# Kernel optimization log

Measured on AMD Instinct MI355X. Metric: run time of the kernel, lower is better.

## Reference

```python
import jax, jax.numpy as jnp
import numpy as np

B, CIN, COUT, N, K = 8, 128, 128, 2000, 16
IN_EPS = 1e-3   # InstanceNorm2d eps in module
BN_EPS = 1e-5   # BatchNorm2d default eps


def conv1x1(x, w, b):
    # x: [B,C,H,W], w: [O,C], b: [O]
    return jnp.einsum('bchw,oc->bohw', x, w) + b[None, :, None, None]


def setup_inputs() -> dict:
    key = jax.random.key(0)
    ks = jax.random.split(key, 12)
    s = 0.05
    return {
        'x_row':   jax.random.normal(ks[0], (B, COUT, N, 1), jnp.float32),
        'x_local': jax.random.normal(ks[1], (B, CIN, N, K), jnp.float32),
        'w0': jax.random.normal(ks[2], (COUT, CIN), jnp.float32) * s,
        'b0': jax.random.normal(ks[3], (COUT,), jnp.float32) * s,
        'bn_g': jnp.ones((COUT,), jnp.float32),
        'bn_b': jnp.zeros((COUT,), jnp.float32),
        'wq': jax.random.normal(ks[4], (COUT, COUT), jnp.float32) * s,
        'bq': jax.random.normal(ks[5], (COUT,), jnp.float32) * s,
        'wk': jax.random.normal(ks[6], (COUT, COUT), jnp.float32) * s,
        'bk': jax.random.normal(ks[7], (COUT,), jnp.float32) * s,
        'wv': jax.random.normal(ks[8], (COUT, COUT), jnp.float32) * s,
        'bv': jax.random.normal(ks[9], (COUT,), jnp.float32) * s,
        'gamma1': jnp.ones((1,), jnp.float32),
    }


def reference(x_row, x_local, w0, b0, bn_g, bn_b, wq, bq, wk, bk, wv, bv, gamma1):
    # att1: Conv1x1 -> InstanceNorm2d(eps=1e-3, no affine) -> BatchNorm2d (train-mode batch stats) -> ReLU
    h = conv1x1(x_local, w0, b0)                       # [B,C,N,K]
    mu = jnp.mean(h, axis=(2, 3), keepdims=True)
    var = jnp.var(h, axis=(2, 3), keepdims=True)
    h = (h - mu) * jax.lax.rsqrt(var + IN_EPS)
    bmu = jnp.mean(h, axis=(0, 2, 3), keepdims=True)
    bvar = jnp.var(h, axis=(0, 2, 3), keepdims=True)
    h = (h - bmu) * jax.lax.rsqrt(bvar + BN_EPS)
    h = h * bn_g[None, :, None, None] + bn_b[None, :, None, None]
    h = jax.nn.relu(h)

    q = conv1x1(h, wq, bq)
    k = conv1x1(h, wk, bk)
    v = conv1x1(h, wv, bv)
    att = jax.nn.softmax(q * k, axis=3)                # softmax over neighbor axis
    out_local = jnp.sum(att * v, axis=3, keepdims=True)  # [B,C,N,1]
    return x_row + gamma1 * out_local
```

## Files before the change

kernel.cpp:

```cpp
#include <hip/hip_runtime.h>
#include <math.h>

#define NB 8
#define NC 128
#define NPOS 2000
#define NK 32000
#define IN_EPS 1e-3f
#define BN_EPS 1e-5f

typedef short bf16x8 __attribute__((ext_vector_type(8)));
typedef _Float16 f16x8 __attribute__((ext_vector_type(8)));
typedef float f32x4 __attribute__((ext_vector_type(4)));
typedef unsigned short ushort_t;
typedef unsigned int uint_t;

#define XSTRIDE 136

#define WSF_SUMP  0
#define WSF_SQP   32768
#define WSF_ALPHA 65536
#define WSF_BETA  66560
#define WSB_WEIGHTS 270336
#define WSB_H     401408
#define WS_NEEDED ((size_t)WSB_H + (size_t)NB * NK * XSTRIDE * 2)

__device__ __forceinline__ f32x4 mfma_bf16(bf16x8 a, bf16x8 b, f32x4 c) {
  return __builtin_amdgcn_mfma_f32_16x16x32_bf16(a, b, c, 0, 0, 0);
}
__device__ __forceinline__ f32x4 mfma_f16(f16x8 a, f16x8 b, f32x4 c) {
  return __builtin_amdgcn_mfma_f32_16x16x32_f16(a, b, c, 0, 0, 0);
}

__device__ __forceinline__ ushort_t f2bf(float f) {
  unsigned u = __float_as_uint(f);
  return (ushort_t)((u + 0x7FFFu + ((u >> 16) & 1u)) >> 16);
}
__device__ __forceinline__ ushort_t f2h(float f) {
  union { _Float16 h; ushort_t u; } cv;
  cv.h = (_Float16)f;
  return cv.u;
}
__device__ __forceinline__ float h2f(ushort_t u) {
  union { _Float16 h; ushort_t u; } cv;
  cv.u = u;
  return (float)cv.h;
}
__device__ __forceinline__ uint_t pk2h(float a, float b) {
  auto h = __builtin_amdgcn_cvt_pkrtz(a, b);
  return __builtin_bit_cast(uint_t, h);
}

template <int ALL_F16>
__global__ __launch_bounds__(256) void k_prep(const float* __restrict__ w0,
    const float* __restrict__ wq, const float* __restrict__ wk,
    const float* __restrict__ wv, ushort_t* __restrict__ wb) {
  int idx = blockIdx.x * 256 + threadIdx.x;
  int m = idx >> 14;
  int e = idx & 16383;
  const float* src = (m == 0) ? w0 : (m == 1) ? wq : (m == 2) ? wk : wv;
  float v = src[e];
  wb[m * 16384 + e] = ALL_F16 ? f2h(v) : f2bf(v);
}

__device__ __forceinline__ void stage_xt128(const float* __restrict__ xb,
                                            ushort_t* __restrict__ xt, int tid) {
  const int col = tid & 127;
  const int hi = tid >> 7;
  const float* p = xb + col;
#pragma unroll
  for (int i = 0; i < 8; ++i) {
    const int c0 = hi * 64 + i * 8;
    ushort_t u[8] __attribute__((aligned(16)));
#pragma unroll
    for (int j = 0; j < 8; ++j) u[j] = f2bf(p[(size_t)(c0 + j) * NK]);
    *(uint4*)(xt + col * XSTRIDE + c0) = *(const uint4*)u;
  }
}

__device__ __forceinline__ void stage_xt64(const float* __restrict__ xb,
                                           ushort_t* __restrict__ xt, int tid) {
  const int col = tid & 63;
  const int hi = tid >> 6;
  const float* p = xb + col;
#pragma unroll
  for (int i = 0; i < 4; ++i) {
    const int c0 = hi * 32 + i * 8;
    ushort_t u[8] __attribute__((aligned(16)));
#pragma unroll
    for (int j = 0; j < 8; ++j) u[j] = f2bf(p[(size_t)(c0 + j) * NK]);
    *(uint4*)(xt + col * XSTRIDE + c0) = *(const uint4*)u;
  }
}

__device__ __forceinline__ void stage_xt64_f16(const float* __restrict__ xb,
                                               ushort_t* __restrict__ xt, int tid) {
  const int col = tid & 63;
  const int hi = tid >> 6;
  const float* p = xb + col;
#pragma unroll
  for (int r = 0; r < 2; ++r) {
    const int c0 = hi * 32 + r * 16;
    float v[16];
#pragma unroll
    for (int j = 0; j < 16; ++j) v[j] = p[(size_t)(c0 + j) * NK];
    uint_t u[8] __attribute__((aligned(16)));
#pragma unroll
    for (int j = 0; j < 8; ++j) u[j] = pk2h(v[2 * j], v[2 * j + 1]);
    *(uint4*)(xt + col * XSTRIDE + c0) = *(const uint4*)u;
    *(uint4*)(xt + col * XSTRIDE + c0 + 8) = *(const uint4*)(u + 4);
  }
}

__global__ __launch_bounds__(256, 6) void k_stats2(const float* __restrict__ x,
    const ushort_t* __restrict__ w0b, float* __restrict__ sumP,
    float* __restrict__ sqP, ushort_t* __restrict__ hg) {
  __shared__ ushort_t xt[64 * XSTRIDE] __attribute__((aligned(16)));
  __shared__ float ssum[128], ssq[128];
  const int b = blockIdx.y;
  const int tid = threadIdx.x;
  stage_xt64_f16(x + (size_t)b * NC * NK + (size_t)blockIdx.x * 64, xt, tid);
  __syncthreads();
  const int lane = tid & 63, w = tid >> 6;
  const int m = lane & 15, quad = lane >> 4;

  uint2 hreg[8];

#pragma unroll
  for (int p = 0; p < 2; ++p) {
    const int ch0 = (w + p * 4) * 16;
    f16x8 wf[4];
#pragma unroll
    for (int kb = 0; kb < 4; ++kb)
      wf[kb] = *(const f16x8*)(w0b + (ch0 + m) * 128 + kb * 32 + quad * 8);
    float s0 = 0.f, s1 = 0.f, s2 = 0.f, s3 = 0.f;
    float q0 = 0.f, q1 = 0.f, q2 = 0.f, q3 = 0.f;
#pragma unroll
    for (int t = 0; t < 4; ++t) {
      const ushort_t* xr = xt + (t * 16 + m) * XSTRIDE;
      f32x4 acc = {0.f, 0.f, 0.f, 0.f};
#pragma unroll
      for (int kb = 0; kb < 4; ++kb) {
        f16x8 bx = *(const f16x8*)(xr + kb * 32 + quad * 8);
        acc = mfma_f16(wf[kb], bx, acc);
      }
      const ushort_t u0 = f2h(acc[0]), u1 = f2h(acc[1]);
      const ushort_t u2 = f2h(acc[2]), u3 = f2h(acc[3]);
      uint2 pk;
      pk.x = (uint_t)u0 | ((uint_t)u1 << 16);
      pk.y = (uint_t)u2 | ((uint_t)u3 << 16);
      hreg[p * 4 + t] = pk;
      const float r0 = h2f(u0), r1 = h2f(u1), r2 = h2f(u2), r3 = h2f(u3);
      s0 += r0; s1 += r1; s2 += r2; s3 += r3;
      q0 = fmaf(r0, r0, q0); q1 = fmaf(r1, r1, q1);
      q2 = fmaf(r2, r2, q2); q3 = fmaf(r3, r3, q3);
    }
#pragma unroll
    for (int d = 1; d < 16; d <<= 1) {
      s0 += __shfl_xor(s0, d); s1 += __shfl_xor(s1, d);
      s2 += __shfl_xor(s2, d); s3 += __shfl_xor(s3, d);
      q0 += __shfl_xor(q0, d); q1 += __shfl_xor(q1, d);
      q2 += __shfl_xor(q2, d); q3 += __shfl_xor(q3, d);
    }
    if (m == 0) {
      ssum[ch0 + quad * 4 + 0] = s0; ssum[ch0 + quad * 4 + 1] = s1;
      ssum[ch0 + quad * 4 + 2] = s2; ssum[ch0 + quad * 4 + 3] = s3;
      ssq[ch0 + quad * 4 + 0] = q0; ssq[ch0 + quad * 4 + 1] = q1;
      ssq[ch0 + quad * 4 + 2] = q2; ssq[ch0 + quad * 4 + 3] = q3;
    }
  }
  __syncthreads();

#pragma unroll
  for (int p = 0; p < 2; ++p) {
    const int ch0 = (w + p * 4) * 16;
#pragma unroll
    for (int t = 0; t < 4; ++t)
      *(uint2*)(xt + (t * 16 + m) * XSTRIDE + ch0 + quad * 4) = hreg[p * 4 + t];
  }
  __syncthreads();

  {
    const uint4* src = (const uint4*)xt;
    uint4* dst =
        (uint4*)(hg + ((size_t)b * NK + (size_t)blockIdx.x * 64) * XSTRIDE);
#pragma unroll
    for (int i = 0; i < 4; ++i) dst[i * 256 + tid] = src[i * 256 + tid];
    if (tid < 64) dst[1024 + tid] = src[1024 + tid];
  }

  if (tid < 128) {
    const int bucket = blockIdx.x & 31;
    atomicAdd(&sumP[bucket * 1024 + b * 128 + tid], ssum[tid]);
    atomicAdd(&sqP[bucket * 1024 + b * 128 + tid], ssq[tid]);
  }
}

__global__ void k_fold(const float* __restrict__ ws_in, const float* __restrict__ bn_g,
                       const float* __restrict__ bn_b, float* __restrict__ alpha,
                       float* __restrict__ beta) {
  int c = threadIdx.x;
  const float* sumP = ws_in + WSF_SUMP;
  const float* sqP = ws_in + WSF_SQP;
  float var[NB], muv[NB];
  float bvar = 0.f;
#pragma unroll 1
  for (int b = 0; b < NB; ++b) {
    float s = 0.f, q = 0.f;
#pragma unroll
    for (int k = 0; k < 32; ++k) {
      s += sumP[k * 1024 + b * 128 + c];
      q += sqP[k * 1024 + b * 128 + c];
    }
    float mu = s * (1.f / NK);
    float v = q * (1.f / NK) - mu * mu;
    muv[b] = mu;
    var[b] = v;
    bvar += v / (v + IN_EPS);
  }
  bvar *= 0.125f;
  float s2 = rsqrtf(bvar + BN_EPS);
  float g = bn_g[c], bb = bn_b[c];
#pragma unroll
  for (int b = 0; b < NB; ++b) {
    float a = rsqrtf(var[b] + IN_EPS) * s2 * g;
    alpha[b * 128 + c] = a;
    beta[b * 128 + c] = bb - muv[b] * a;
  }
}

__device__ __forceinline__ uint_t norm2(uint_t hv, float a0, float a1, float c0,
                                        float c1) {
  float lo = h2f((ushort_t)(hv & 0xffffu));
  float hi = h2f((ushort_t)(hv >> 16));
  return pk2h(fmaxf(fmaf(lo, a0, c0), 0.f), fmaxf(fmaf(hi, a1, c1), 0.f));
}

__global__ __launch_bounds__(256, 6) void k_fused2(
    const ushort_t* __restrict__ hg, const float* __restrict__ x_row,
    const ushort_t* __restrict__ wb, const float* __restrict__ alpha,
    const float* __restrict__ beta, const float* __restrict__ bq,
    const float* __restrict__ bk, const float* __restrict__ bv,
    const float* __restrict__ g1p, float* __restrict__ out) {
  __shared__ ushort_t xt[64 * XSTRIDE] __attribute__((aligned(16)));
  __shared__ float souts[128 * 5];
  const int b = blockIdx.y;
  const int tid = threadIdx.x;
  const int lane = tid & 63, w = tid >> 6;

  const size_t oi = ((size_t)b * NC + tid) * NPOS + blockIdx.x * 4;
  float4 xr_early;
  if (tid < 128) xr_early = *(const float4*)(x_row + oi);

  {
    const uint4* src =
        (const uint4*)(hg + ((size_t)b * NK + (size_t)blockIdx.x * 64) * XSTRIDE);
    uint4* dst = (uint4*)xt;
    const float* ap = alpha + b * 128;
    const float* bp = beta + b * 128;
#pragma unroll
    for (int i = 0; i < 5; ++i) {
      if (i < 4 || tid < 64) {
        const int j = i * 256 + tid;
        uint4 v = src[j];
        const int c = j % 17;
        if (c < 16) {
          const int ch = c * 8;
          const float4 a0 = *(const float4*)(ap + ch);
          const float4 a1 = *(const float4*)(ap + ch + 4);
          const float4 c0 = *(const float4*)(bp + ch);
          const float4 c1 = *(const float4*)(bp + ch + 4);
          v.x = norm2(v.x, a0.x, a0.y, c0.x, c0.y);
          v.y = norm2(v.y, a0.z, a0.w, c0.z, c0.w);
          v.z = norm2(v.z, a1.x, a1.y, c1.x, c1.y);
          v.w = norm2(v.w, a1.z, a1.w, c1.z, c1.w);
        }
        dst[j] = v;
      }
    }
  }
  const float g1 = g1p[0];
  __syncthreads();

  const int m = lane & 15, quad = lane >> 4;
  const ushort_t* wqb = wb + 16384;
  const ushort_t* wkb = wb + 32768;
  const ushort_t* wvb = wb + 49152;
#pragma unroll 1
  for (int p = 0; p < 2; ++p) {
    const int ch0 = (w + p * 4) * 16;
    f16x8 wqf[4], wkf[4], wvf[4];
#pragma unroll
    for (int kb = 0; kb < 4; ++kb) {
      wqf[kb] = *(const f16x8*)(wqb + (ch0 + m) * 128 + kb * 32 + quad * 8);
      wkf[kb] = *(const f16x8*)(wkb + (ch0 + m) * 128 + kb * 32 + quad * 8);
      wvf[kb] = *(const f16x8*)(wvb + (ch0 + m) * 128 + kb * 32 + quad * 8);
    }
    const float bqv = bq[ch0 + m];
    const float bkv = bk[ch0 + m];
    const float bvv = bv[ch0 + m];
#pragma unroll 1
    for (int t = 0; t < 4; ++t) {
      const ushort_t* hr = xt + (t * 16 + m) * XSTRIDE;
      f16x8 af[4];
#pragma unroll
      for (int kb = 0; kb < 4; ++kb)
        af[kb] = *(const f16x8*)(hr + kb * 32 + quad * 8);
      f32x4 qa = {0.f, 0.f, 0.f, 0.f};
      f32x4 ka = {0.f, 0.f, 0.f, 0.f};
#pragma unroll
      for (int kb = 0; kb < 4; ++kb) qa = mfma_f16(af[kb], wqf[kb], qa);
#pragma unroll
      for (int kb = 0; kb < 4; ++kb) ka = mfma_f16(af[kb], wkf[kb], ka);
      float p0 = (qa[0] + bqv) * (ka[0] + bkv);
      float p1 = (qa[1] + bqv) * (ka[1] + bkv);
      float p2 = (qa[2] + bqv) * (ka[2] + bkv);
      float p3 = (qa[3] + bqv) * (ka[3] + bkv);
      float mx = fmaxf(fmaxf(p0, p1), fmaxf(p2, p3));
      mx = fmaxf(mx, __shfl_xor(mx, 16));
      mx = fmaxf(mx, __shfl_xor(mx, 32));
      float e0 = __expf(p0 - mx), e1 = __expf(p1 - mx);
      float e2 = __expf(p2 - mx), e3 = __expf(p3 - mx);
      float sm = (e0 + e1) + (e2 + e3);
      sm += __shfl_xor(sm, 16);
      sm += __shfl_xor(sm, 32);
      f32x4 va = {0.f, 0.f, 0.f, 0.f};
#pragma unroll
      for (int kb = 0; kb < 4; ++kb) va = mfma_f16(af[kb], wvf[kb], va);
      float r0 = e0 * va[0] + e1 * va[1] + e2 * va[2] + e3 * va[3];
      r0 += __shfl_xor(r0, 16);
      r0 += __shfl_xor(r0, 32);
      if (quad == 0) souts[(ch0 + m) * 5 + t] = r0 / sm + bvv;
    }
  }
  __syncthreads();

  if (tid < 128) {
    const float* sp = souts + tid * 5;
    float4 o;
    o.x = xr_early.x + g1 * sp[0];
    o.y = xr_early.y + g1 * sp[1];
    o.z = xr_early.z + g1 * sp[2];
    o.w = xr_early.w + g1 * sp[3];
    *(float4*)(out + oi) = o;
  }
}

__global__ __launch_bounds__(256, 4) void k_stats1(const float* __restrict__ x,
    const ushort_t* __restrict__ w0b, float* __restrict__ sumP,
    float* __restrict__ sqP) {
  __shared__ ushort_t xt[128 * XSTRIDE];
  __shared__ float ssum[128], ssq[128];
  const int b = blockIdx.y;
  const int tid = threadIdx.x;
  stage_xt128(x + (size_t)b * NC * NK + (size_t)blockIdx.x * 128, xt, tid);
  __syncthreads();
  const int lane = tid & 63, w = tid >> 6;
  const int m = lane & 15, quad = lane >> 4;

#pragma unroll 1
  for (int p = 0; p < 2; ++p) {
    const int ch0 = (w + p * 4) * 16;
    bf16x8 wf[4];
#pragma unroll
    for (int kb = 0; kb < 4; ++kb)
      wf[kb] = *(const bf16x8*)(w0b + (ch0 + m) * 128 + kb * 32 + quad * 8);
    float s = 0.f, q2 = 0.f;
#pragma unroll 2
    for (int t = 0; t < 8; ++t) {
      const ushort_t* xr = xt + (t * 16 + m) * XSTRIDE;
      f32x4 acc = {0.f, 0.f, 0.f, 0.f};
#pragma unroll
      for (int kb = 0; kb < 4; ++kb) {
        bf16x8 af = *(const bf16x8*)(xr + kb * 32 + quad * 8);
        acc = mfma_bf16(af, wf[kb], acc);
      }
      s += (acc[0] + acc[1]) + (acc[2] + acc[3]);
      q2 += (acc[0] * acc[0] + acc[1] * acc[1]) +
            (acc[2] * acc[2] + acc[3] * acc[3]);
    }
    s += __shfl_xor(s, 16);
    s += __shfl_xor(s, 32);
    q2 += __shfl_xor(q2, 16);
    q2 += __shfl_xor(q2, 32);
    if (quad == 0) {
      ssum[ch0 + m] = s;
      ssq[ch0 + m] = q2;
    }
  }
  __syncthreads();
  if (tid < 128) {
    const int bucket = blockIdx.x & 31;
    atomicAdd(&sumP[bucket * 1024 + b * 128 + tid], ssum[tid]);
    atomicAdd(&sqP[bucket * 1024 + b * 128 + tid], ssq[tid]);
  }
}

__global__ __launch_bounds__(256, 4) void k_fused1(const float* __restrict__ x,
    const float* __restrict__ x_row, const ushort_t* __restrict__ wb,
    const float* __restrict__ alpha, const float* __restrict__ beta,
    const float* __restrict__ bq, const float* __restrict__ bk,
    const float* __restrict__ bv, const float* __restrict__ g1p,
    float* __restrict__ out) {
  __shared__ ushort_t xt[64 * XSTRIDE];
  __shared__ ushort_t ht[64 * XSTRIDE];
  __shared__ float souts[128 * 5];
  const int b = blockIdx.y;
  const int tid = threadIdx.x;
  stage_xt64(x + (size_t)b * NC * NK + (size_t)blockIdx.x * 64, xt, tid);
  const float g1 = g1p[0];
  __syncthreads();
  const int lane = tid & 63, w = tid >> 6;
  const int m = lane & 15, quad = lane >> 4;
  const ushort_t* w0b = wb;
  const ushort_t* wqb = wb + 16384;
  const ushort_t* wkb = wb + 32768;
  const ushort_t* wvb = wb + 49152;

#pragma unroll 1
  for (int p = 0; p < 2; ++p) {
    const int ch0 = (w + p * 4) * 16;
    bf16x8 wf[4];
#pragma unroll
    for (int kb = 0; kb < 4; ++kb)
      wf[kb] = *(const bf16x8*)(w0b + (ch0 + m) * 128 + kb * 32 + quad * 8);
    const float4 av = *(const float4*)(alpha + b * 128 + ch0 + quad * 4);
    const float4 bev = *(const float4*)(beta + b * 128 + ch0 + quad * 4);
#pragma unroll
    for (int t = 0; t < 4; ++t) {
      const ushort_t* xr = xt + (t * 16 + m) * XSTRIDE;
      f32x4 acc = {0.f, 0.f, 0.f, 0.f};
#pragma unroll
      for (int kb = 0; kb < 4; ++kb) {
        bf16x8 bx = *(const bf16x8*)(xr + kb * 32 + quad * 8);
        acc = mfma_bf16(wf[kb], bx, acc);
      }
      float h0 = fmaxf(acc[0] * av.x + bev.x, 0.f);
      float h1 = fmaxf(acc[1] * av.y + bev.y, 0.f);
      float h2 = fmaxf(acc[2] * av.z + bev.z, 0.f);
      float h3 = fmaxf(acc[3] * av.w + bev.w, 0.f);
      uint2 pk;
      pk.x = (uint_t)f2bf(h0) | ((uint_t)f2bf(h1) << 16);
      pk.y = (uint_t)f2bf(h2) | ((uint_t)f2bf(h3) << 16);
      *(uint2*)(ht + (t * 16 + m) * XSTRIDE + ch0 + quad * 4) = pk;
    }
  }
  __syncthreads();

#pragma unroll 1
  for (int p = 0; p < 2; ++p) {
    const int ch0 = (w + p * 4) * 16;
    bf16x8 wqf[4], wkf[4], wvf[4];
#pragma unroll
    for (int kb = 0; kb < 4; ++kb) {
      wqf[kb] = *(const bf16x8*)(wqb + (ch0 + m) * 128 + kb * 32 + quad * 8);
      wkf[kb] = *(const bf16x8*)(wkb + (ch0 + m) * 128 + kb * 32 + quad * 8);
      wvf[kb] = *(const bf16x8*)(wvb + (ch0 + m) * 128 + kb * 32 + quad * 8);
    }
    const float bqv = bq[ch0 + m];
    const float bkv = bk[ch0 + m];
    const float bvv = bv[ch0 + m];
#pragma unroll 1
    for (int t = 0; t < 4; ++t) {
      const ushort_t* hr = ht + (t * 16 + m) * XSTRIDE;
      bf16x8 af[4];
#pragma unroll
      for (int kb = 0; kb < 4; ++kb)
        af[kb] = *(const bf16x8*)(hr + kb * 32 + quad * 8);
      f32x4 qa = {0.f, 0.f, 0.f, 0.f};
      f32x4 ka = {0.f, 0.f, 0.f, 0.f};
#pragma unroll
      for (int kb = 0; kb < 4; ++kb) qa = mfma_bf16(af[kb], wqf[kb], qa);
#pragma unroll
      for (int kb = 0; kb < 4; ++kb) ka = mfma_bf16(af[kb], wkf[kb], ka);
      float p0 = (qa[0] + bqv) * (ka[0] + bkv);
      float p1 = (qa[1] + bqv) * (ka[1] + bkv);
      float p2 = (qa[2] + bqv) * (ka[2] + bkv);
      float p3 = (qa[3] + bqv) * (ka[3] + bkv);
      float mx = fmaxf(fmaxf(p0, p1), fmaxf(p2, p3));
      mx = fmaxf(mx, __shfl_xor(mx, 16));
      mx = fmaxf(mx, __shfl_xor(mx, 32));
      float e0 = __expf(p0 - mx), e1 = __expf(p1 - mx);
      float e2 = __expf(p2 - mx), e3 = __expf(p3 - mx);
      float sm = (e0 + e1) + (e2 + e3);
      sm += __shfl_xor(sm, 16);
      sm += __shfl_xor(sm, 32);
      f32x4 va = {0.f, 0.f, 0.f, 0.f};
#pragma unroll
      for (int kb = 0; kb < 4; ++kb) va = mfma_bf16(af[kb], wvf[kb], va);
      float r0 = e0 * (va[0] + bvv) + e1 * (va[1] + bvv) +
                 e2 * (va[2] + bvv) + e3 * (va[3] + bvv);
      r0 += __shfl_xor(r0, 16);
      r0 += __shfl_xor(r0, 32);
      if (quad == 0) souts[(ch0 + m) * 5 + t] = r0 / sm;
    }
  }
  __syncthreads();

  if (tid < 128) {
    const int c = tid;
    const size_t oi = ((size_t)b * NC + c) * NPOS + blockIdx.x * 4;
    const float4 xr = *(const float4*)(x_row + oi);
    const float* sp = souts + c * 5;
    float4 o;
    o.x = xr.x + g1 * sp[0];
    o.y = xr.y + g1 * sp[1];
    o.z = xr.z + g1 * sp[2];
    o.w = xr.w + g1 * sp[3];
    *(float4*)(out + oi) = o;
  }
}

extern "C" void kernel_launch(void* const* d_in, const int* in_sizes, int n_in,
                              void* d_out, int out_size, void* d_ws, size_t ws_size,
                              hipStream_t stream) {
  (void)in_sizes; (void)n_in; (void)out_size;
  const float* x_row   = (const float*)d_in[0];
  const float* x_local = (const float*)d_in[1];
  const float* w0   = (const float*)d_in[2];
  const float* bn_g = (const float*)d_in[4];
  const float* bn_b = (const float*)d_in[5];
  const float* wq   = (const float*)d_in[6];
  const float* bq   = (const float*)d_in[7];
  const float* wk   = (const float*)d_in[8];
  const float* bk   = (const float*)d_in[9];
  const float* wv   = (const float*)d_in[10];
  const float* bv   = (const float*)d_in[11];
  const float* gamma1 = (const float*)d_in[12];
  float* out = (float*)d_out;
  float* ws = (float*)d_ws;
  ushort_t* wb = (ushort_t*)((char*)d_ws + WSB_WEIGHTS);
  ushort_t* hg = (ushort_t*)((char*)d_ws + WSB_H);

  (void)hipMemsetAsync(ws, 0, 65536 * sizeof(float), stream);

  if (ws_size >= WS_NEEDED) {
    k_prep<1><<<256, 256, 0, stream>>>(w0, wq, wk, wv, wb);
    k_stats2<<<dim3(500, NB), 256, 0, stream>>>(x_local, wb, ws + WSF_SUMP,
                                                ws + WSF_SQP, hg);
    k_fold<<<1, 128, 0, stream>>>(ws, bn_g, bn_b, ws + WSF_ALPHA, ws + WSF_BETA);
    k_fused2<<<dim3(500, NB), 256, 0, stream>>>(hg, x_row, wb, ws + WSF_ALPHA,
                                                ws + WSF_BETA, bq, bk, bv, gamma1,
                                                out);
  } else {
    k_prep<0><<<256, 256, 0, stream>>>(w0, wq, wk, wv, wb);
    k_stats1<<<dim3(250, NB), 256, 0, stream>>>(x_local, wb, ws + WSF_SUMP,
                                                ws + WSF_SQP);
    k_fold<<<1, 128, 0, stream>>>(ws, bn_g, bn_b, ws + WSF_ALPHA, ws + WSF_BETA);
    k_fused1<<<dim3(500, NB), 256, 0, stream>>>(x_local, x_row, wb, ws + WSF_ALPHA,
                                                ws + WSF_BETA, bq, bk, bv, gamma1,
                                                out);
  }
}
```

Before: 332.7 us.

## Process two position tiles per block with register-prefetched second tile

Replaces k_fused2 with k_fused3, which handles 8 positions per block instead of 4, halving the grid. Both tiles of h are loaded into registers at the start, and the second tile is normalized and stored to a separate LDS buffer after the first tile's QKV/softmax phase. The aim is to hide global-load latency behind MFMA work and amortize per-block setup such as the x_row load and weight fragments. In exchange, register and LDS use go up, launch bounds drop from 6 to 4 blocks per CU, and there are fewer blocks to spread across CUs.

```diff
diff --git a/kernel.cpp b/kernel.cpp
--- a/kernel.cpp
+++ b/kernel.cpp
@@ -15,6 +15,7 @@
 typedef unsigned int uint_t;
 
 #define XSTRIDE 136
+#define SOUTS 9
 
 #define WSF_SUMP  0
 #define WSF_SQP   32768
@@ -235,56 +236,44 @@
   return pk2h(fmaxf(fmaf(lo, a0, c0), 0.f), fmaxf(fmaf(hi, a1, c1), 0.f));
 }
 
-__global__ __launch_bounds__(256, 6) void k_fused2(
-    const ushort_t* __restrict__ hg, const float* __restrict__ x_row,
-    const ushort_t* __restrict__ wb, const float* __restrict__ alpha,
-    const float* __restrict__ beta, const float* __restrict__ bq,
-    const float* __restrict__ bk, const float* __restrict__ bv,
-    const float* __restrict__ g1p, float* __restrict__ out) {
-  __shared__ ushort_t xt[64 * XSTRIDE] __attribute__((aligned(16)));
-  __shared__ float souts[128 * 5];
-  const int b = blockIdx.y;
-  const int tid = threadIdx.x;
-  const int lane = tid & 63, w = tid >> 6;
-
-  const size_t oi = ((size_t)b * NC + tid) * NPOS + blockIdx.x * 4;
-  float4 xr_early;
-  if (tid < 128) xr_early = *(const float4*)(x_row + oi);
-
-  {
-    const uint4* src =
-        (const uint4*)(hg + ((size_t)b * NK + (size_t)blockIdx.x * 64) * XSTRIDE);
-    uint4* dst = (uint4*)xt;
-    const float* ap = alpha + b * 128;
-    const float* bp = beta + b * 128;
-#pragma unroll
-    for (int i = 0; i < 5; ++i) {
-      if (i < 4 || tid < 64) {
-        const int j = i * 256 + tid;
-        uint4 v = src[j];
-        const int c = j % 17;
-        if (c < 16) {
-          const int ch = c * 8;
-          const float4 a0 = *(const float4*)(ap + ch);
-          const float4 a1 = *(const float4*)(ap + ch + 4);
-          const float4 c0 = *(const float4*)(bp + ch);
-          const float4 c1 = *(const float4*)(bp + ch + 4);
-          v.x = norm2(v.x, a0.x, a0.y, c0.x, c0.y);
-          v.y = norm2(v.y, a0.z, a0.w, c0.z, c0.w);
-          v.z = norm2(v.z, a1.x, a1.y, c1.x, c1.y);
-          v.w = norm2(v.w, a1.z, a1.w, c1.z, c1.w);
-        }
-        dst[j] = v;
+__device__ __forceinline__ void tile_load(const uint4* __restrict__ src, int tid,
+                                          uint4 v[5]) {
+#pragma unroll
+  for (int i = 0; i < 4; ++i) v[i] = src[i * 256 + tid];
+  if (tid < 64) v[4] = src[1024 + tid];
+}
+
+__device__ __forceinline__ void tile_norm_store(const uint4 v[5],
+                                                ushort_t* __restrict__ xt, int tid,
+                                                const float* __restrict__ ap,
+                                                const float* __restrict__ bp) {
+#pragma unroll
+  for (int i = 0; i < 5; ++i) {
+    if (i < 4 || tid < 64) {
+      const int j = i * 256 + tid;
+      uint4 t = v[i];
+      const int c = j % 17;
+      if (c < 16) {
+        const int ch = c * 8;
+        const float4 a0 = *(const float4*)(ap + ch);
+        const float4 a1 = *(const float4*)(ap + ch + 4);
+        const float4 c0 = *(const float4*)(bp + ch);
+        const float4 c1 = *(const float4*)(bp + ch + 4);
+        t.x = norm2(t.x, a0.x, a0.y, c0.x, c0.y);
+        t.y = norm2(t.y, a0.z, a0.w, c0.z, c0.w);
+        t.z = norm2(t.z, a1.x, a1.y, c1.x, c1.y);
+        t.w = norm2(t.w, a1.z, a1.w, c1.z, c1.w);
       }
-    }
-  }
-  const float g1 = g1p[0];
-  __syncthreads();
-
-  const int m = lane & 15, quad = lane >> 4;
-  const ushort_t* wqb = wb + 16384;
-  const ushort_t* wkb = wb + 32768;
-  const ushort_t* wvb = wb + 49152;
+      ((uint4*)xt)[j] = t;
+    }
+  }
+}
+
+__device__ __forceinline__ void qkv_phase(const ushort_t* __restrict__ xt,
+    float* __restrict__ souts, const ushort_t* __restrict__ wqb,
+    const ushort_t* __restrict__ wkb, const ushort_t* __restrict__ wvb,
+    const float* __restrict__ bq, const float* __restrict__ bk,
+    const float* __restrict__ bv, int w, int m, int quad, int tbase) {
 #pragma unroll 1
   for (int p = 0; p < 2; ++p) {
     const int ch0 = (w + p * 4) * 16;
@@ -329,19 +318,70 @@
       float r0 = e0 * va[0] + e1 * va[1] + e2 * va[2] + e3 * va[3];
       r0 += __shfl_xor(r0, 16);
       r0 += __shfl_xor(r0, 32);
-      if (quad == 0) souts[(ch0 + m) * 5 + t] = r0 / sm + bvv;
-    }
-  }
-  __syncthreads();
-
+      if (quad == 0) souts[(ch0 + m) * SOUTS + tbase + t] = r0 / sm + bvv;
+    }
+  }
+}
+
+__global__ __launch_bounds__(256, 4) void k_fused3(
+    const ushort_t* __restrict__ hg, const float* __restrict__ x_row,
+    const ushort_t* __restrict__ wb, const float* __restrict__ alpha,
+    const float* __restrict__ beta, const float* __restrict__ bq,
+    const float* __restrict__ bk, const float* __restrict__ bv,
+    const float* __restrict__ g1p, float* __restrict__ out) {
+  __shared__ ushort_t xtA[64 * XSTRIDE] __attribute__((aligned(16)));
+  __shared__ ushort_t xtB[64 * XSTRIDE] __attribute__((aligned(16)));
+  __shared__ float souts[128 * SOUTS];
+  const int b = blockIdx.y;
+  const int tid = threadIdx.x;
+  const int lane = tid & 63, w = tid >> 6;
+  const int m = lane & 15, quad = lane >> 4;
+
+  const size_t oi = ((size_t)b * NC + tid) * NPOS + (size_t)blockIdx.x * 8;
+  float4 xr0, xr1;
   if (tid < 128) {
-    const float* sp = souts + tid * 5;
-    float4 o;
-    o.x = xr_early.x + g1 * sp[0];
-    o.y = xr_early.y + g1 * sp[1];
-    o.z = xr_early.z + g1 * sp[2];
-    o.w = xr_early.w + g1 * sp[3];
-    *(float4*)(out + oi) = o;
+    xr0 = *(const float4*)(x_row + oi);
+    xr1 = *(const float4*)(x_row + oi + 4);
+  }
+
+  const uint4* srcA =
+      (const uint4*)(hg + ((size_t)b * NK + (size_t)blockIdx.x * 128) * XSTRIDE);
+  const uint4* srcB = srcA + 1088;
+  uint4 vA[5], vB[5];
+  tile_load(srcA, tid, vA);
+  tile_load(srcB, tid, vB);
+
+  const float* ap = alpha + b * 128;
+  const float* bp = beta + b * 128;
+  tile_norm_store(vA, xtA, tid, ap, bp);
+  const float g1 = g1p[0];
+  __syncthreads();
+
+  const ushort_t* wqb = wb + 16384;
+  const ushort_t* wkb = wb + 32768;
+  const ushort_t* wvb = wb + 49152;
+
+  qkv_phase(xtA, souts, wqb, wkb, wvb, bq, bk, bv, w, m, quad, 0);
+
+  tile_norm_store(vB, xtB, tid, ap, bp);
+  __syncthreads();
+
+  qkv_phase(xtB, souts, wqb, wkb, wvb, bq, bk, bv, w, m, quad, 4);
+  __syncthreads();
+
+  if (tid < 128) {
+    const float* sp = souts + tid * SOUTS;
+    float4 o0, o1;
+    o0.x = xr0.x + g1 * sp[0];
+    o0.y = xr0.y + g1 * sp[1];
+    o0.z = xr0.z + g1 * sp[2];
+    o0.w = xr0.w + g1 * sp[3];
+    o1.x = xr1.x + g1 * sp[4];
+    o1.y = xr1.y + g1 * sp[5];
+    o1.z = xr1.z + g1 * sp[6];
+    o1.w = xr1.w + g1 * sp[7];
+    *(float4*)(out + oi) = o0;
+    *(float4*)(out + oi + 4) = o1;
   }
 }
 
@@ -538,7 +578,7 @@
     k_stats2<<<dim3(500, NB), 256, 0, stream>>>(x_local, wb, ws + WSF_SUMP,
                                                 ws + WSF_SQP, hg);
     k_fold<<<1, 128, 0, stream>>>(ws, bn_g, bn_b, ws + WSF_ALPHA, ws + WSF_BETA);
-    k_fused2<<<dim3(500, NB), 256, 0, stream>>>(hg, x_row, wb, ws + WSF_ALPHA,
+    k_fused3<<<dim3(250, NB), 256, 0, stream>>>(hg, x_row, wb, ws + WSF_ALPHA,
                                                 ws + WSF_BETA, bq, bk, bv, gamma1,
                                                 out);
   } else {
```

After: 319.1 us. 4.1% less time.
